# Kernel tuning notes

Measured on AMD Instinct MI355X. Metric: run time of the kernel, lower is better.

Reference implementation:

```python
import jax, jax.numpy as jnp
import numpy as np

H = 128          # hidden_size
GX = GY = 512    # grid_size
SW = 2           # spatial_width
NX = GX + 3 * SW # memory extent x (as in SpatialExternalMemory ctor)
NY = GY + 3 * SW
B = 512          # batch (num trajectories)
T = 64           # seq len (recurrent steps)


def setup_inputs() -> dict:
    key = jax.random.key(0)
    ks = jax.random.split(key, 9)
    stdv = 1.0 / np.sqrt(H)
    feat = jax.random.normal(ks[0], (B, T, 2), jnp.float32)
    # integer grid coords stored as floats in cols 2:4 (cast to long in forward)
    coords = jax.random.randint(ks[1], (B, T, 2), 0, GX).astype(jnp.float32)
    feature_tensor = jnp.concatenate([feat, coords], axis=-1)  # [B, T, 4]
    seq_lengths = jax.random.randint(ks[2], (B,), 1, T + 1)
    uni = lambda k, shp: jax.random.uniform(k, shp, jnp.float32, -stdv, stdv)
    return {
        "feature_tensor": feature_tensor,
        "W_ih": uni(ks[3], (4 * H, 2)),
        "b_ih": uni(ks[4], (4 * H,)),
        "W_hh": uni(ks[5], (4 * H, H)),
        "b_hh": uni(ks[6], (4 * H,)),
        "W_out": uni(ks[7], (H, 2 * H)),   # Attention.linear_out: [H, 2H]
        "b_out": uni(ks[8], (H,)),
        "seq_lengths": seq_lengths,
    }


def reference(feature_tensor, W_ih, b_ih, W_hh, b_hh, W_out, b_out, seq_lengths):
    step_idx = jnp.maximum(seq_lengths.astype(jnp.int32), 1) - 1  # [B]
    offsets = jnp.arange(-SW, SW + 1)                              # [K], K=2*SW+1
    K = 2 * SW + 1
    memory0 = jnp.zeros((NX, NY, H), jnp.float32)
    hidden0 = jnp.zeros((B, H), jnp.float32)
    last0 = jnp.zeros((B, H), jnp.float32)

    def step(carry, inp):
        hidden, memory, last = carry
        xt, t = inp                                 # xt: [B,4]
        feat = xt[:, :2]
        grid = xt[:, 2:4].astype(jnp.int32) + SW    # [B,2]
        gi = feat @ W_ih.T + b_ih                   # [B,4H]
        gh = hidden @ W_hh.T + b_hh                 # [B,4H]
        i_r, i_i, i_n, i_s = jnp.split(gi, 4, axis=1)
        h_r, h_i, h_n, h_s = jnp.split(gh, 4, axis=1)
        resetgate = jax.nn.sigmoid(i_r + h_r)
        updategate = jax.nn.sigmoid(i_i + h_i)
        spatialgate = jax.nn.sigmoid(i_s + h_s)
        newgate = jnp.tanh(i_n + resetgate * h_n)
        # --- find_nearby_grids: 5x5 neighborhood gather ---
        gx = jnp.clip(grid[:, 0], 0, NX - 1)
        gy = jnp.clip(grid[:, 1], 0, NY - 1)
        xi = jnp.clip(gx[:, None] + offsets[None, :], 0, NX - 1)   # [B,K]
        yi = jnp.clip(gy[:, None] + offsets[None, :], 0, NY - 1)   # [B,K]
        xg = jnp.broadcast_to(xi[:, :, None], (B, K, K)).reshape(B, K * K)
        yg = jnp.broadcast_to(yi[:, None, :], (B, K, K)).reshape(B, K * K)
        context = memory[xg, yg]                    # [B, K*K, H]
        # --- Attention(newgate.detach(), context) ---
        q = jax.lax.stop_gradient(newgate)
        scores = jnp.einsum('bh,bkh->bk', q, context)
        scores = jnp.where(scores == 0.0, -jnp.inf, scores)
        attn = jax.nn.softmax(scores, axis=1)
        attn = jnp.where(jnp.isnan(attn), 0.0, attn)
        mix = jnp.einsum('bk,bkh->bh', attn, context)
        atten_cs = jnp.tanh(jnp.concatenate([mix, q], axis=-1) @ W_out.T + b_out)
        curr = newgate + spatialgate * atten_cs
        out = curr + updategate * (hidden - curr)
        # --- in-cell memory write (detached, training-mode path) ---
        sd = jax.lax.stop_gradient(spatialgate)
        od = jax.lax.stop_gradient(out)
        upd = sd * memory[gx, gy] + (1.0 - sd) * od
        memory = memory.at[gx, gy].set(upd)
        last = jnp.where((step_idx == t)[:, None], out, last)
        return (out, memory, last), None

    xs = (jnp.swapaxes(feature_tensor, 0, 1), jnp.arange(T))
    (_, _, last), _ = jax.lax.scan(step, (hidden0, memory0, last0), xs)
    return last
```

## Files before the change

kernel.cpp:

```cpp
#include <hip/hip_runtime.h>
#include <hip/hip_fp16.h>
#include <math.h>

#define Hc   128
#define Bc   512
#define Tc   64
#define NXc  518
#define NCELL (518*518)
#define NEV  (Bc*Tc)
#define SWc  2


__global__ void k_build(const float* __restrict__ feat, int* __restrict__ head,
                        int* __restrict__ nxt, int* __restrict__ cellxy) {
    int gid = blockIdx.x * 256 + threadIdx.x;
    if (gid >= NEV) return;
    int b = gid >> 6, t = gid & 63;
    int base = (b * Tc + t) * 4;
    int gx = (int)feat[base + 2] + SWc;
    int gy = (int)feat[base + 3] + SWc;
    gx = min(max(gx, 0), NXc - 1);
    gy = min(max(gy, 0), NXc - 1);
    int cell = gx * NXc + gy;
    int e = t * Bc + b;
    cellxy[e] = (gx << 16) | gy;
    int old = atomicExch(&head[cell], e);
    nxt[e] = old;
}

__global__ void k_resolve(const int* __restrict__ head, const int* __restrict__ nxt,
                          const int* __restrict__ cellxy, int* __restrict__ dep) {
    int gid = blockIdx.x * 256 + threadIdx.x;
    if (gid >= NEV * 25) return;
    int r = gid / 25, k = gid - r * 25;
    int t = r & 63, b = r >> 6;
    int e0 = t * Bc + b;
    int xy = cellxy[e0];
    int gx = xy >> 16, gy = xy & 0xffff;
    int cx = gx + (k / 5) - SWc, cy = gy + (k % 5) - SWc;
    cx = min(max(cx, 0), NXc - 1);
    cy = min(max(cy, 0), NXc - 1);
    int cell = cx * NXc + cy;
    int best = -1;
    for (int e = head[cell]; e >= 0; e = nxt[e])
        if ((e >> 9) < t && e > best) best = e;
    dep[r * 25 + k] = best;
}


#define LOG2E 1.4426950408889634f
__device__ __forceinline__ float fexp(float x)  { return __builtin_amdgcn_exp2f(x * LOG2E); }
__device__ __forceinline__ float fsig(float x)  { return __builtin_amdgcn_rcpf(1.f + fexp(-x)); }
__device__ __forceinline__ float ftanh(float x) { return 1.f - 2.f * __builtin_amdgcn_rcpf(1.f + fexp(2.f * x)); }

template <int CTRL>
__device__ __forceinline__ float dppadd(float x) {
    int t = __builtin_amdgcn_update_dpp(0, __float_as_int(x), CTRL, 0xF, 0xF, true);
    return x + __int_as_float(t);
}
template <int CTRL>
__device__ __forceinline__ float dppmax(float x) {
    int t = __builtin_amdgcn_update_dpp(0, __float_as_int(x), CTRL, 0xF, 0xF, true);
    return fmaxf(x, __int_as_float(t));
}
__device__ __forceinline__ float swz16(float x) {
    return __int_as_float(__builtin_amdgcn_ds_swizzle(__float_as_int(x), 0x401F));
}
__device__ __forceinline__ float redsum64(float d) {
    d = dppadd<0xB1>(d); d = dppadd<0x4E>(d);
    d = dppadd<0x141>(d); d = dppadd<0x140>(d);
    d += swz16(d);
    d += __shfl_xor(d, 32, 64);
    return d;
}
__device__ __forceinline__ float redsum8(float d) {
    d = dppadd<0xB1>(d); d = dppadd<0x4E>(d); d = dppadd<0x141>(d);
    return d;
}

__device__ __forceinline__ void barlds() {
    asm volatile("" ::: "memory");
    __builtin_amdgcn_s_waitcnt(0xC07F);
    __builtin_amdgcn_s_barrier();
    asm volatile("" ::: "memory");
}

__device__ __forceinline__ unsigned flagload(const unsigned* p) {
    return __hip_atomic_load(p, __ATOMIC_RELAXED, __HIP_MEMORY_SCOPE_AGENT);
}


constexpr int LDS_FLOATS = 256 + 1024 + 256 + 256 + 64 + 2048 + 512 + 16 + 256 + 128;
constexpr int LDS_BYTES  = LDS_FLOATS * 4;

__global__ void
__attribute__((amdgpu_flat_work_group_size(1024, 1024)))
__attribute__((amdgpu_waves_per_eu(4, 4)))
step_main(const float* __restrict__ feat, const float* __restrict__ Wih,
          const float* __restrict__ bih,  const float* __restrict__ Whh,
          const float* __restrict__ bhh,  const float* __restrict__ Wout,
          const float* __restrict__ bout, const int*   __restrict__ seq,
          const int*   __restrict__ dep,  float* __restrict__ vbuf,
          unsigned*    __restrict__ flags, float* __restrict__ dout) {
    extern __shared__ float lds[];
    float* hid   = lds;
    float* g     = hid   + 256;
    float* gin   = g     + 1024;
    float* ctr   = gin   + 256;
    float* scor  = ctr   + 256;
    float* pmix  = scor  + 64;
    float* catL  = pmix  + 2048;
    float* fxy   = catL  + 512;
    float* updL  = fxy   + 16;
    int*   depv  = (int*)(updL + 256);

    const int tid  = threadIdx.x;
    const int blk  = blockIdx.x;
    const int lane = tid & 63;
    const int w    = tid >> 6;
    const int wj   = w >> 3;
    const int ww   = w & 7;

    const int grp = tid >> 3;
    const int s   = tid & 7;
    float4 wrr[4][4];
    {
        const float4* wb = (const float4*)Whh;
        #pragma unroll
        for (int r = 0; r < 4; ++r)
            #pragma unroll
            for (int i = 0; i < 4; ++i)
                wrr[r][i] = wb[(size_t)(4 * grp + r) * 32 + s + 8 * i];
    }
    #pragma unroll
    for (int r = 0; r < 4; ++r)
        #pragma unroll
        for (int i = 0; i < 4; ++i)
            asm volatile("" : "+v"(wrr[r][i].x), "+v"(wrr[r][i].y),
                              "+v"(wrr[r][i].z), "+v"(wrr[r][i].w));

    const int jwl = s >> 2;
    const int rwl = 4 * grp + (s & 3);
    const float bihr = bih[rwl], bhhr = bhh[rwl];
    const float wihA = Wih[rwl * 2 + 0], wihB = Wih[rwl * 2 + 1];
    const int chunk = rwl >> 7;

    const int oo7 = tid & 127, rep7 = tid >> 7;
    unsigned wo[16];
    {
        const float* wrow = Wout + (size_t)oo7 * 256 + rep7 * 32;
        #pragma unroll
        for (int m = 0; m < 16; ++m) {
            __half2 hh = __floats2half2_rn(wrow[2 * m], wrow[2 * m + 1]);
            unsigned u; __builtin_memcpy(&u, &hh, 4);
            wo[m] = u;
            asm volatile("" : "+v"(wo[m]));
        }
    }
    const float boutr = bout[oo7];

    if (tid < 256) hid[tid] = 0.f;
    if (tid < 8) { int j = tid >> 2, c = tid & 3;
                   fxy[tid] = feat[((size_t)(blk * 2 + j) * Tc + 0) * 4 + c]; }
    if (tid < 50) {
        int j = (tid >= 25), k = tid - j * 25;
        depv[tid] = dep[(((size_t)(blk * 2 + j)) * Tc + 0) * 25 + k];
    }
    const int s0 = max(seq[blk * 2 + 0], 1) - 1;
    const int s1 = max(seq[blk * 2 + 1], 1) - 1;
    __syncthreads();

    const float NEG_INF = -__builtin_inff();

    for (int t = 0; t < Tc; ++t) {
        const float* fx = fxy + (t & 1) * 8;
        int* depvCur = depv + (t & 1) * 64;
        int* depvNxt = depv + ((t + 1) & 1) * 64;

        if (t > 0 && (w == 0 || w == 2)) {
            int j = w >> 1;
            float2 u = *(const float2*)&updL[j * 128 + 2 * lane];
            unsigned long long raw; __builtin_memcpy(&raw, &u, 8);
            __hip_atomic_store((unsigned long long*)(vbuf +
                ((size_t)((t - 1) * Bc + blk * 2 + j)) * Hc + 2 * lane),
                raw, __ATOMIC_RELAXED, __HIP_MEMORY_SCOPE_AGENT);
        }
        const int mye = (lane < 25) ? depvCur[wj * 25 + lane] : -1;
        unsigned fpre = 1u;
        if (mye >= 0)
            fpre = flagload(&flags[mye]);

        float acc[2][4];
        #pragma unroll
        for (int j = 0; j < 2; ++j) {
            const float4* hp = (const float4*)(hid + j * 128);
            float4 h0 = hp[s], h1 = hp[s + 8], h2 = hp[s + 16], h3 = hp[s + 24];
            #pragma unroll
            for (int r = 0; r < 4; ++r) {
                float4 w0 = wrr[r][0], w1 = wrr[r][1], w2 = wrr[r][2], w3 = wrr[r][3];
                float a = 0.f;
                a = fmaf(w0.x, h0.x, fmaf(w0.y, h0.y, fmaf(w0.z, h0.z, fmaf(w0.w, h0.w, a))));
                a = fmaf(w1.x, h1.x, fmaf(w1.y, h1.y, fmaf(w1.z, h1.z, fmaf(w1.w, h1.w, a))));
                a = fmaf(w2.x, h2.x, fmaf(w2.y, h2.y, fmaf(w2.z, h2.z, fmaf(w2.w, h2.w, a))));
                a = fmaf(w3.x, h3.x, fmaf(w3.y, h3.y, fmaf(w3.z, h3.z, fmaf(w3.w, h3.w, a))));
                acc[j][r] = a;
            }
        }
        #pragma unroll
        for (int j = 0; j < 2; ++j)
            #pragma unroll
            for (int r = 0; r < 4; ++r)
                acc[j][r] = redsum8(acc[j][r]);
        {
            int sb = s & 3;
            float m0 = (sb == 0) ? acc[0][0] : (sb == 1) ? acc[0][1]
                     : (sb == 2) ? acc[0][2] : acc[0][3];
            float m1 = (sb == 0) ? acc[1][0] : (sb == 1) ? acc[1][1]
                     : (sb == 2) ? acc[1][2] : acc[1][3];
            float mine = jwl ? m1 : m0;
            float gi = fmaf(wihA, fx[jwl * 4 + 0], wihB * fx[jwl * 4 + 1]);
            g[jwl * 512 + rwl] = mine + bhhr + ((chunk == 2) ? 0.f : (gi + bihr));
            if (chunk == 2) gin[jwl * 128 + (rwl & 127)] = gi + bihr;
        }
        if (tid >= 512 && tid < 562 && t + 1 < Tc) {
            int idx = tid - 512;
            int j = (idx >= 25), k = idx - j * 25;
            depvNxt[idx] = dep[(((size_t)(blk * 2 + j)) * Tc + (t + 1)) * 25 + k];
        }
        if (tid >= 960 && tid < 968 && t + 1 < Tc) {
            int idx = tid - 960, j = idx >> 2, c = idx & 3;
            fxy[((t + 1) & 1) * 8 + idx] =
                feat[((size_t)(blk * 2 + j) * Tc + (t + 1)) * 4 + c];
        }
        if (t > 0 && (w == 0 || w == 2)) {
            asm volatile("s_waitcnt vmcnt(0)" ::: "memory");
            if (lane == 0)
                __hip_atomic_store(&flags[(t - 1) * Bc + blk * 2 + (w >> 1)], 1u,
                                   __ATOMIC_RELAXED, __HIP_MEMORY_SCOPE_AGENT);
        }
        {
            bool pend = (mye >= 0) && (fpre == 0u);
            while (__any(pend)) {
                if (pend && flagload(&flags[mye]) != 0u)
                    pend = false;
                if (__any(pend)) __builtin_amdgcn_s_sleep(1);
            }
        }
        asm volatile("" ::: "memory");
        float2 valk[4];
        int    evk[4];
        #pragma unroll
        for (int kk = 0; kk < 4; ++kk) {
            int k = ww + 8 * kk;
            evk[kk] = (k < 25) ? depvCur[wj * 25 + k] : -1;
            valk[kk] = make_float2(0.f, 0.f);
            if (evk[kk] >= 0)
                valk[kk] = *(const float2*)(vbuf + (size_t)evk[kk] * Hc + 2 * lane);
        }
        barlds();

        float q0, q1;
        {
            float2 gr2 = *(const float2*)&g[wj * 512 + 2 * lane];
            float2 gn2 = *(const float2*)&g[wj * 512 + 256 + 2 * lane];
            float2 gi2 = *(const float2*)&gin[wj * 128 + 2 * lane];
            q0 = ftanh(gi2.x + fsig(gr2.x) * gn2.x);
            q1 = ftanh(gi2.y + fsig(gr2.y) * gn2.y);
        }
        if (ww == 0) *(float2*)&catL[wj * 256 + 128 + 2 * lane] = make_float2(q0, q1);
        if (ww == 1) *(float2*)&catL[wj * 256 + 2 * lane] = make_float2(0.f, 0.f);
        if (ww == 4)
            *(float2*)&ctr[wj * 128 + 2 * lane] =
                (evk[1] >= 0) ? valk[1] : make_float2(0.f, 0.f);
        #pragma unroll
        for (int kk = 0; kk < 4; ++kk) {
            int k = ww + 8 * kk;
            if (k < 25) {
                float sc;
                if (evk[kk] >= 0) {
                    float d = fmaf(valk[kk].x, q0, valk[kk].y * q1);
                    d = redsum64(d);
                    sc = (d == 0.f) ? NEG_INF : d;
                } else sc = NEG_INF;
                if (lane == 0) scor[wj * 32 + k] = sc;
            }
        }
        barlds();

        {
            int k2 = lane & 31;
            float v = (k2 < 25) ? scor[wj * 32 + k2] : NEG_INF;
            float m = v;
            m = dppmax<0xB1>(m); m = dppmax<0x4E>(m);
            m = dppmax<0x141>(m); m = dppmax<0x140>(m);
            m = fmaxf(m, swz16(m));
            float a = 0.f;
            if (m != NEG_INF) {
                float p = (v == NEG_INF) ? 0.f : fexp(v - m);
                float ssum = p;
                ssum = dppadd<0xB1>(ssum); ssum = dppadd<0x4E>(ssum);
                ssum = dppadd<0x141>(ssum); ssum = dppadd<0x140>(ssum);
                ssum += swz16(ssum);
                a = p / ssum;
            }
            if ((evk[0] >= 0) | (evk[1] >= 0) | (evk[2] >= 0) | (evk[3] >= 0)) {
                float pm0 = 0.f, pm1 = 0.f;
                #pragma unroll
                for (int kk = 0; kk < 4; ++kk) {
                    int k = ww + 8 * kk;
                    if (k < 25 && evk[kk] >= 0) {
                        float ak = __int_as_float(
                            __builtin_amdgcn_readlane(__float_as_int(a), k));
                        pm0 = fmaf(ak, valk[kk].x, pm0);
                        pm1 = fmaf(ak, valk[kk].y, pm1);
                    }
                }
                atomicAdd(&catL[wj * 256 + 2 * lane],     pm0);
                atomicAdd(&catL[wj * 256 + 2 * lane + 1], pm1);
            }
        }
        barlds();

        {
            const float4* c04 = (const float4*)(catL + rep7 * 32);
            const float4* c14 = (const float4*)(catL + 256 + rep7 * 32);
            float acc0 = 0.f, acc1 = 0.f;
            #pragma unroll
            for (int i = 0; i < 8; ++i) {
                unsigned ua = wo[2 * i], ub = wo[2 * i + 1];
                __half2 wa, wb2;
                __builtin_memcpy(&wa, &ua, 4); __builtin_memcpy(&wb2, &ub, 4);
                float wx = __low2float(wa), wy = __high2float(wa);
                float wz = __low2float(wb2), wv = __high2float(wb2);
                float4 c0 = c04[i], c1 = c14[i];
                acc0 = fmaf(wx, c0.x, fmaf(wy, c0.y, fmaf(wz, c0.z, fmaf(wv, c0.w, acc0))));
                acc1 = fmaf(wx, c1.x, fmaf(wy, c1.y, fmaf(wz, c1.z, fmaf(wv, c1.w, acc1))));
            }
            pmix[rep7 * 128 + oo7]       = acc0;
            pmix[(8 + rep7) * 128 + oo7] = acc1;
        }
        barlds();

        if (tid < 256) {
            int j = tid >> 7, h = tid & 127;
            float tot = boutr;
            #pragma unroll
            for (int p = 0; p < 8; ++p) tot += pmix[(j * 8 + p) * 128 + h];
            float at = ftanh(tot);
            float gr = g[j * 512 + h],       gu = g[j * 512 + 128 + h];
            float gn = g[j * 512 + 256 + h], gs = g[j * 512 + 384 + h];
            float rr = fsig(gr), uu = fsig(gu), ss = fsig(gs);
            float nn = ftanh(gin[j * 128 + h] + rr * gn);
            float hv = hid[j * 128 + h];
            float curr = fmaf(ss, at, nn);
            float outv = curr + uu * (hv - curr);
            hid[j * 128 + h] = outv;
            if (t < Tc - 1)
                updL[tid] = fmaf(ss, ctr[j * 128 + h], (1.f - ss) * outv);
            int sj = (j == 0) ? s0 : s1;
            if (sj == t) dout[(size_t)(blk * 2 + j) * Hc + h] = outv;
        }
        barlds();
    }
}


extern "C" void kernel_launch(void* const* d_in, const int* in_sizes, int n_in,
                              void* d_out, int out_size, void* d_ws, size_t ws_size,
                              hipStream_t stream) {
    const float* feat = (const float*)d_in[0];
    const float* Wih  = (const float*)d_in[1];
    const float* bih  = (const float*)d_in[2];
    const float* Whh  = (const float*)d_in[3];
    const float* bhh  = (const float*)d_in[4];
    const float* Wout = (const float*)d_in[5];
    const float* bout = (const float*)d_in[6];
    const int*   seq  = (const int*)d_in[7];

    char* ws = (char*)d_ws;
    size_t off = 0;
    auto carve = [&](size_t bytes) { char* p = ws + off; off += (bytes + 511) & ~(size_t)511; return p; };
    float*    vbuf   = (float*)   carve((size_t)NEV * Hc * 4);
    int*      head   = (int*)     carve((size_t)NCELL * 4);
    int*      nxt    = (int*)     carve((size_t)NEV * 4);
    int*      cellxy = (int*)     carve((size_t)NEV * 4);
    int*      dep    = (int*)     carve((size_t)NEV * 25 * 4);
    unsigned* flags  = (unsigned*)carve((size_t)NEV * 4);

    hipMemsetAsync(head, 0xFF, (size_t)NCELL * 4, stream);
    hipMemsetAsync(flags, 0, (size_t)NEV * 4, stream);

    k_build<<<(NEV + 255) / 256, 256, 0, stream>>>(feat, head, nxt, cellxy);
    k_resolve<<<(NEV * 25 + 255) / 256, 256, 0, stream>>>(head, nxt, cellxy, dep);

    hipFuncSetAttribute((const void*)step_main,
                        hipFuncAttributeMaxDynamicSharedMemorySize, LDS_BYTES);
    step_main<<<256, 1024, LDS_BYTES, stream>>>(feat, Wih, bih, Whh, bhh, Wout, bout,
                                                seq, dep, vbuf, flags, (float*)d_out);
}
```

Baseline: 486.0 us.

## Replace LDS atomics with partial-sum buffer and in-wave DPP reduction for output projection

Attention mix partials are now written to a per-wave LDS buffer and summed in a separate pass, replacing the LDS atomicAdd accumulation. The output projection is remapped so that each wave owns 8 output rows, with the 8 column chunks split across lanes. The partial products are reduced inside the wave using DPP, swizzle and shuffle, which lets the final GRU update run without an extra LDS round-trip. This trades the atomics and one barrier-separated reduction phase for an added reduction pass and cross-lane ops, and the final update now runs on only 8 lanes per wave.

```diff
diff --git a/kernel.cpp b/kernel.cpp
--- a/kernel.cpp
+++ b/kernel.cpp
@@ -90,7 +90,7 @@
 }
 
 
-constexpr int LDS_FLOATS = 256 + 1024 + 256 + 256 + 64 + 2048 + 512 + 16 + 256 + 128;
+constexpr int LDS_FLOATS = 256 + 1024 + 256 + 256 + 256 + 64 + 2048 + 512 + 16 + 256 + 128;
 constexpr int LDS_BYTES  = LDS_FLOATS * 4;
 
 __global__ void
@@ -107,7 +107,8 @@
     float* g     = hid   + 256;
     float* gin   = g     + 1024;
     float* ctr   = gin   + 256;
-    float* scor  = ctr   + 256;
+    float* qvL   = ctr   + 256;
+    float* scor  = qvL   + 256;
     float* pmix  = scor  + 64;
     float* catL  = pmix  + 2048;
     float* fxy   = catL  + 512;
@@ -145,10 +146,11 @@
     const float wihA = Wih[rwl * 2 + 0], wihB = Wih[rwl * 2 + 1];
     const int chunk = rwl >> 7;
 
-    const int oo7 = tid & 127, rep7 = tid >> 7;
+    const int oi = lane & 7, p = lane >> 3;
+    const int oo = 8 * w + oi;
     unsigned wo[16];
     {
-        const float* wrow = Wout + (size_t)oo7 * 256 + rep7 * 32;
+        const float* wrow = Wout + (size_t)oo * 256 + p * 32;
         #pragma unroll
         for (int m = 0; m < 16; ++m) {
             __half2 hh = __floats2half2_rn(wrow[2 * m], wrow[2 * m + 1]);
@@ -157,7 +159,7 @@
             asm volatile("" : "+v"(wo[m]));
         }
     }
-    const float boutr = bout[oo7];
+    const float boutr = bout[oo];
 
     if (tid < 256) hid[tid] = 0.f;
     if (tid < 8) { int j = tid >> 2, c = tid & 3;
@@ -267,8 +269,7 @@
             q0 = ftanh(gi2.x + fsig(gr2.x) * gn2.x);
             q1 = ftanh(gi2.y + fsig(gr2.y) * gn2.y);
         }
-        if (ww == 0) *(float2*)&catL[wj * 256 + 128 + 2 * lane] = make_float2(q0, q1);
-        if (ww == 1) *(float2*)&catL[wj * 256 + 2 * lane] = make_float2(0.f, 0.f);
+        if (ww == 0) *(float2*)&qvL[wj * 128 + 2 * lane] = make_float2(q0, q1);
         if (ww == 4)
             *(float2*)&ctr[wj * 128 + 2 * lane] =
                 (evk[1] >= 0) ? valk[1] : make_float2(0.f, 0.f);
@@ -296,69 +297,75 @@
             m = fmaxf(m, swz16(m));
             float a = 0.f;
             if (m != NEG_INF) {
-                float p = (v == NEG_INF) ? 0.f : fexp(v - m);
-                float ssum = p;
+                float pr = (v == NEG_INF) ? 0.f : fexp(v - m);
+                float ssum = pr;
                 ssum = dppadd<0xB1>(ssum); ssum = dppadd<0x4E>(ssum);
                 ssum = dppadd<0x141>(ssum); ssum = dppadd<0x140>(ssum);
                 ssum += swz16(ssum);
-                a = p / ssum;
-            }
-            if ((evk[0] >= 0) | (evk[1] >= 0) | (evk[2] >= 0) | (evk[3] >= 0)) {
-                float pm0 = 0.f, pm1 = 0.f;
-                #pragma unroll
-                for (int kk = 0; kk < 4; ++kk) {
-                    int k = ww + 8 * kk;
-                    if (k < 25 && evk[kk] >= 0) {
-                        float ak = __int_as_float(
-                            __builtin_amdgcn_readlane(__float_as_int(a), k));
-                        pm0 = fmaf(ak, valk[kk].x, pm0);
-                        pm1 = fmaf(ak, valk[kk].y, pm1);
-                    }
+                a = pr / ssum;
+            }
+            float pm0 = 0.f, pm1 = 0.f;
+            #pragma unroll
+            for (int kk = 0; kk < 4; ++kk) {
+                int k = ww + 8 * kk;
+                if (k < 25 && evk[kk] >= 0) {
+                    float ak = __int_as_float(
+                        __builtin_amdgcn_readlane(__float_as_int(a), k));
+                    pm0 = fmaf(ak, valk[kk].x, pm0);
+                    pm1 = fmaf(ak, valk[kk].y, pm1);
                 }
-                atomicAdd(&catL[wj * 256 + 2 * lane],     pm0);
-                atomicAdd(&catL[wj * 256 + 2 * lane + 1], pm1);
-            }
+            }
+            *(float2*)&pmix[(wj * 8 + ww) * 128 + 2 * lane] = make_float2(pm0, pm1);
         }
         barlds();
 
+        if (tid < 256) {
+            int j = tid >> 7, h = tid & 127;
+            float mix = 0.f;
+            #pragma unroll
+            for (int pp = 0; pp < 8; ++pp) mix += pmix[(j * 8 + pp) * 128 + h];
+            catL[j * 256 + h] = mix;
+            catL[j * 256 + 128 + h] = qvL[j * 128 + h];
+        }
+        barlds();
+
         {
-            const float4* c04 = (const float4*)(catL + rep7 * 32);
-            const float4* c14 = (const float4*)(catL + 256 + rep7 * 32);
+            const float4* cat4 = (const float4*)catL;
             float acc0 = 0.f, acc1 = 0.f;
             #pragma unroll
-            for (int i = 0; i < 8; ++i) {
-                unsigned ua = wo[2 * i], ub = wo[2 * i + 1];
+            for (int c = 0; c < 8; ++c) {
+                int cc = (c + p) & 7;
+                unsigned ua = wo[2 * cc], ub = wo[2 * cc + 1];
                 __half2 wa, wb2;
                 __builtin_memcpy(&wa, &ua, 4); __builtin_memcpy(&wb2, &ub, 4);
                 float wx = __low2float(wa), wy = __high2float(wa);
                 float wz = __low2float(wb2), wv = __high2float(wb2);
-                float4 c0 = c04[i], c1 = c14[i];
-                acc0 = fmaf(wx, c0.x, fmaf(wy, c0.y, fmaf(wz, c0.z, fmaf(wv, c0.w, acc0))));
-                acc1 = fmaf(wx, c1.x, fmaf(wy, c1.y, fmaf(wz, c1.z, fmaf(wv, c1.w, acc1))));
-            }
-            pmix[rep7 * 128 + oo7]       = acc0;
-            pmix[(8 + rep7) * 128 + oo7] = acc1;
-        }
-        barlds();
-
-        if (tid < 256) {
-            int j = tid >> 7, h = tid & 127;
-            float tot = boutr;
-            #pragma unroll
-            for (int p = 0; p < 8; ++p) tot += pmix[(j * 8 + p) * 128 + h];
-            float at = ftanh(tot);
-            float gr = g[j * 512 + h],       gu = g[j * 512 + 128 + h];
-            float gn = g[j * 512 + 256 + h], gs = g[j * 512 + 384 + h];
-            float rr = fsig(gr), uu = fsig(gu), ss = fsig(gs);
-            float nn = ftanh(gin[j * 128 + h] + rr * gn);
-            float hv = hid[j * 128 + h];
-            float curr = fmaf(ss, at, nn);
-            float outv = curr + uu * (hv - curr);
-            hid[j * 128 + h] = outv;
-            if (t < Tc - 1)
-                updL[tid] = fmaf(ss, ctr[j * 128 + h], (1.f - ss) * outv);
-            int sj = (j == 0) ? s0 : s1;
-            if (sj == t) dout[(size_t)(blk * 2 + j) * Hc + h] = outv;
+                float4 v0 = cat4[p * 8 + cc];
+                float4 v1 = cat4[64 + p * 8 + cc];
+                acc0 = fmaf(wx, v0.x, fmaf(wy, v0.y, fmaf(wz, v0.z, fmaf(wv, v0.w, acc0))));
+                acc1 = fmaf(wx, v1.x, fmaf(wy, v1.y, fmaf(wz, v1.z, fmaf(wv, v1.w, acc1))));
+            }
+            acc0 = dppadd<0x128>(acc0); acc0 += swz16(acc0); acc0 += __shfl_xor(acc0, 32, 64);
+            acc1 = dppadd<0x128>(acc1); acc1 += swz16(acc1); acc1 += __shfl_xor(acc1, 32, 64);
+            if (lane < 8) {
+                #pragma unroll
+                for (int j = 0; j < 2; ++j) {
+                    float tot = ((j == 0) ? acc0 : acc1) + boutr;
+                    float at = ftanh(tot);
+                    float gr = g[j * 512 + oo],       gu = g[j * 512 + 128 + oo];
+                    float gn = g[j * 512 + 256 + oo], gs = g[j * 512 + 384 + oo];
+                    float rr = fsig(gr), uu = fsig(gu), ss = fsig(gs);
+                    float nn = ftanh(gin[j * 128 + oo] + rr * gn);
+                    float hv = hid[j * 128 + oo];
+                    float curr = fmaf(ss, at, nn);
+                    float outv = curr + uu * (hv - curr);
+                    hid[j * 128 + oo] = outv;
+                    if (t < Tc - 1)
+                        updL[j * 128 + oo] = fmaf(ss, ctr[j * 128 + oo], (1.f - ss) * outv);
+                    int sj = (j == 0) ? s0 : s1;
+                    if (sj == t) dout[(size_t)(blk * 2 + j) * Hc + oo] = outv;
+                }
+            }
         }
         barlds();
     }
```

Measured after the change: 447.5 us. 1.09x faster.
